# Performance work log

Measured on AMD Instinct MI355X. Metric: run time of the kernel, lower is better.

The kernel has to match this reference:

```python
import jax, jax.numpy as jnp
import numpy as np

D_MODEL = 1024
NUM_HEADS = 16
D_K = D_MODEL // NUM_HEADS


def setup_inputs() -> dict:
    key = jax.random.key(0)
    ks = jax.random.split(key, 3)
    B, S = 4, 2048
    x = jax.random.normal(ks[0], (B, S, D_MODEL), dtype=jnp.float32)
    mask = jnp.ones((1, 1, S, S), dtype=jnp.int32)
    # xavier-uniform-ish init for weights, zeros for biases (matches _reset_parameters)
    lim_qkv = float(np.sqrt(6.0 / (D_MODEL + 3 * D_MODEL)))
    w_qkv = jax.random.uniform(ks[1], (D_MODEL, 3 * D_MODEL), minval=-lim_qkv, maxval=lim_qkv, dtype=jnp.float32)
    b_qkv = jnp.zeros((3 * D_MODEL,), dtype=jnp.float32)
    lim_out = float(np.sqrt(6.0 / (2 * D_MODEL)))
    w_out = jax.random.uniform(ks[2], (D_MODEL, D_MODEL), minval=-lim_out, maxval=lim_out, dtype=jnp.float32)
    b_out = jnp.zeros((D_MODEL,), dtype=jnp.float32)
    return {"x": x, "mask": mask, "w_qkv": w_qkv, "b_qkv": b_qkv, "w_out": w_out, "b_out": b_out}


def reference(x, mask, w_qkv, b_qkv, w_out, b_out):
    B, S, _ = x.shape
    qkv = x @ w_qkv + b_qkv                      # [B,S,3D]
    q, k, v = jnp.split(qkv, 3, axis=-1)         # each [B,S,D]

    def split_heads(t):
        return t.reshape(B, S, NUM_HEADS, D_K).transpose(0, 2, 1, 3)  # [B,H,S,Dk]

    q, k, v = split_heads(q), split_heads(k), split_heads(v)
    scores = jnp.einsum('bhqd,bhkd->bhqk', q, k) / jnp.sqrt(jnp.float32(D_K))
    scores = jnp.where(mask == 0, jnp.float32(-jnp.inf), scores)
    attn = jax.nn.softmax(scores, axis=-1)
    out = jnp.einsum('bhqk,bhkd->bhqd', attn, v)  # [B,H,S,Dk]
    out = out.transpose(0, 2, 1, 3).reshape(B, S, D_MODEL)
    return out @ w_out + b_out
```

## Files before the change

### kernel.cpp

```cpp
#include <hip/hip_runtime.h>
#include <hip/hip_bf16.h>

typedef __bf16 bf16x8 __attribute__((ext_vector_type(8)));
typedef float f32x4 __attribute__((ext_vector_type(4)));
typedef unsigned int u32x4 __attribute__((ext_vector_type(4)));
typedef unsigned short u16;
typedef unsigned int u32;

__device__ __forceinline__ u16 f2bf(float f) {
    union { float f; u32 u; } v; v.f = f;
    u32 r = v.u + 0x7fffu + ((v.u >> 16) & 1u);
    return (u16)(r >> 16);
}

__device__ __forceinline__ u32 cvtpk(float lo, float hi) {
    u32 r;
    asm("v_cvt_pk_bf16_f32 %0, %1, %2" : "=v"(r) : "v"(lo), "v"(hi));
    return r;
}

__device__ __forceinline__ void swap16(u32& a, u32& b) {
    asm("v_permlane16_swap_b32 %0, %1" : "+v"(a), "+v"(b));
}
__device__ __forceinline__ void swap32(u32& a, u32& b) {
    asm("v_permlane32_swap_b32 %0, %1" : "+v"(a), "+v"(b));
}

#define MFMA(a, b, c) __builtin_amdgcn_mfma_f32_16x16x32_bf16((a), (b), (c), 0, 0, 0)

#define GLOAD16(g, l)                                                          \
    __builtin_amdgcn_global_load_lds(                                          \
        (const __attribute__((address_space(1))) u32*)(g),                     \
        (__attribute__((address_space(3))) u32*)(l), 16, 0, 0)

#define QSCALE 0.18033688011112042f

__global__ __launch_bounds__(256) void k_transpose_w(const float* __restrict__ src,
                                                     u16* __restrict__ dst, int K, int N) {
    __shared__ float tile[32][33];
    int n0 = blockIdx.x * 32, k0 = blockIdx.y * 32;
    int tx = threadIdx.x, ty = threadIdx.y;
#pragma unroll
    for (int i = 0; i < 4; i++)
        tile[ty + i * 8][tx] = src[(k0 + ty + i * 8) * N + n0 + tx];
    __syncthreads();
#pragma unroll
    for (int i = 0; i < 4; i++)
        dst[(n0 + ty + i * 8) * K + k0 + tx] = f2bf(tile[tx][ty + i * 8]);
}

__global__ __launch_bounds__(256) void k_cvt_x(const float* __restrict__ X,
                                               u16* __restrict__ Xb) {
    int i = blockIdx.x * 256 + threadIdx.x;
    float4 a = *(const float4*)&X[i * 8];
    float4 b = *(const float4*)&X[i * 8 + 4];
    uint4 o;
    o.x = cvtpk(a.x, a.y);
    o.y = cvtpk(a.z, a.w);
    o.z = cvtpk(b.x, b.y);
    o.w = cvtpk(b.z, b.w);
    *(uint4*)&Xb[i * 8] = o;
}

__global__ __launch_bounds__(256) void k_gemm_qkv(const u16* __restrict__ Xb,
                                                  const u16* __restrict__ Wt,
                                                  const float* __restrict__ bias,
                                                  u16* __restrict__ Qb,
                                                  u16* __restrict__ Kb,
                                                  u16* __restrict__ Vt) {
    __shared__ __align__(16) u16 Asw[128 * 64];
    __shared__ __align__(16) u16 Bsw[128 * 64];
    const int K = 1024;
    int m0 = blockIdx.x * 128, n0 = blockIdx.y * 128;
    int tid = threadIdx.x, lane = tid & 63, w = tid >> 6;
    int wm = w >> 1, wn = w & 1;
    int l15 = lane & 15, l4 = lane >> 4;

    f32x4 z = {0.f, 0.f, 0.f, 0.f};
    f32x4 acc[4][4];
#pragma unroll
    for (int i = 0; i < 4; i++)
#pragma unroll
        for (int j = 0; j < 4; j++) acc[i][j] = z;

    for (int kt = 0; kt < K / 64; kt++) {
#pragma unroll
        for (int it = 0; it < 4; it++) {
            int c = tid + it * 256;
            int row = c >> 3, g = (c & 7) ^ (row & 7);
            GLOAD16(&Xb[(m0 + row) * K + kt * 64 + g * 8], &Asw[(c & ~63) * 8]);
            GLOAD16(&Wt[(n0 + row) * K + kt * 64 + g * 8], &Bsw[(c & ~63) * 8]);
        }
        __syncthreads();
#pragma unroll
        for (int ks = 0; ks < 2; ks++) {
            bf16x8 af[4], bfr[4];
#pragma unroll
            for (int mt = 0; mt < 4; mt++) {
                int row = wm * 64 + mt * 16 + l15;
                af[mt] = *(const bf16x8*)&Asw[row * 64 + ((ks * 4 + l4) ^ (row & 7)) * 8];
            }
#pragma unroll
            for (int nt = 0; nt < 4; nt++) {
                int row = wn * 64 + nt * 16 + l15;
                bfr[nt] = *(const bf16x8*)&Bsw[row * 64 + ((ks * 4 + l4) ^ (row & 7)) * 8];
            }
#pragma unroll
            for (int mt = 0; mt < 4; mt++)
#pragma unroll
                for (int nt = 0; nt < 4; nt++)
                    acc[mt][nt] = MFMA(af[mt], bfr[nt], acc[mt][nt]);
        }
        __syncthreads();
    }
    int part = n0 >> 10;
#pragma unroll
    for (int nt = 0; nt < 4; nt++) {
        int col = n0 + wn * 64 + nt * 16 + l15;
        float bv = bias[col];
        int cc = col & 1023, h = cc >> 6, dk = cc & 63;
        if (part == 2) {
#pragma unroll
            for (int mt = 0; mt < 4; mt++) {
                int row = m0 + wm * 64 + mt * 16 + l4 * 4;
                int b = row >> 11, s = row & 2047;
                uint2 pk;
                pk.x = cvtpk(acc[mt][nt][0] + bv, acc[mt][nt][1] + bv);
                pk.y = cvtpk(acc[mt][nt][2] + bv, acc[mt][nt][3] + bv);
                *(uint2*)&Vt[((b * 16 + h) * 64 + dk) * 2048 + s] = pk;
            }
        } else {
            u16* dst = (part == 0) ? Qb : Kb;
            float sc = (part == 0) ? QSCALE : 1.0f;
#pragma unroll
            for (int mt = 0; mt < 4; mt++) {
#pragma unroll
                for (int q = 0; q < 4; q++) {
                    int row = m0 + wm * 64 + mt * 16 + l4 * 4 + q;
                    int b = row >> 11, s = row & 2047;
                    float v = (acc[mt][nt][q] + bv) * sc;
                    dst[((b * 16 + h) * 2048 + s) * 64 + dk] = f2bf(v);
                }
            }
        }
    }
}

__global__ __launch_bounds__(512) void k_attn(const u16* __restrict__ Qb,
                                              const u16* __restrict__ Kb,
                                              const u16* __restrict__ Vt,
                                              u16* __restrict__ Ob) {
    __shared__ __align__(16) u16 Ksw[2 * 128 * 64];
    __shared__ __align__(16) u16 Vsw[2 * 128 * 64];
    const int S = 2048;
    int bid = blockIdx.x;
    int nbid = (bid & 7) * 64 + (bid >> 3);
    int bh = nbid >> 3;
    int qblk = nbid & 7;
    int b = bh >> 4, h = bh & 15;
    int tid = threadIdx.x, lane = tid & 63, w = tid >> 6;
    int l15 = lane & 15, l4 = lane >> 4, l7 = l15 & 7;
    int q0 = qblk * 256 + w * 32;

    const u16* KbB = Kb + bh * S * 64;
    const u16* VtB = Vt + bh * 64 * S;

    bf16x8 qf[2][2];
#pragma unroll
    for (int mt = 0; mt < 2; mt++)
#pragma unroll
        for (int ks = 0; ks < 2; ks++)
            qf[mt][ks] = *(const bf16x8*)&Qb[(bh * S + q0 + mt * 16 + l15) * 64 + ks * 32 + l4 * 8];

    const f32x4 z = {0.f, 0.f, 0.f, 0.f};
    f32x4 o[2][4];
    f32x4 ol[2];
#pragma unroll
    for (int mt = 0; mt < 2; mt++) {
        ol[mt] = z;
#pragma unroll
        for (int nt = 0; nt < 4; nt++) o[mt][nt] = z;
    }
    union { u32x4 u; bf16x8 bb; } onesu;
    onesu.u = (u32x4){0x3F803F80u, 0x3F803F80u, 0x3F803F80u, 0x3F803F80u};
    const bf16x8 onesf = onesu.bb;

    auto stage = [&](int buf, int kv0) {
#pragma unroll
        for (int it = 0; it < 2; it++) {
            int c = tid + it * 512;
            {
                int row = c >> 3, g = (c & 7) ^ (row & 7);
                GLOAD16(&KbB[(kv0 + row) * 64 + g * 8], &Ksw[buf * 8192 + (c & ~63) * 8]);
            }
            {
                int half = c >> 9, row = (c >> 3) & 63, g = (c & 7) ^ (row & 7);
                GLOAD16(&VtB[row * S + kv0 + half * 64 + g * 8], &Vsw[buf * 8192 + (c & ~63) * 8]);
            }
        }
    };

    stage(0, 0);
    __syncthreads();

    for (int kv = 0; kv < S / 128; kv++) {
        int cur = kv & 1;
        if (kv + 1 < S / 128) stage(cur ^ 1, (kv + 1) * 128);
        const u16* Kc = &Ksw[cur * 8192];
        const u16* Vc = &Vsw[cur * 8192];

#pragma unroll
        for (int half = 0; half < 2; half++) {
            const u16* Kh = Kc + half * 4096;
            const u16* Vh = Vc + half * 4096;

            f32x4 sa[2][4];
            __builtin_amdgcn_s_setprio(1);
            {
                bf16x8 kf[4];
#pragma unroll
                for (int nt = 0; nt < 4; nt++)
                    kf[nt] = *(const bf16x8*)&Kh[(nt * 16 + l15) * 64 + (l4 ^ l7) * 8];
#pragma unroll
                for (int mt = 0; mt < 2; mt++)
#pragma unroll
                    for (int nt = 0; nt < 4; nt++)
                        sa[mt][nt] = MFMA(kf[nt], qf[mt][0], z);
#pragma unroll
                for (int nt = 0; nt < 4; nt++)
                    kf[nt] = *(const bf16x8*)&Kh[(nt * 16 + l15) * 64 + ((4 + l4) ^ l7) * 8];
#pragma unroll
                for (int mt = 0; mt < 2; mt++)
#pragma unroll
                    for (int nt = 0; nt < 4; nt++)
                        sa[mt][nt] = MFMA(kf[nt], qf[mt][1], sa[mt][nt]);
            }
            __builtin_amdgcn_s_setprio(0);

            bf16x8 pf[2][2];
#pragma unroll
            for (int mt = 0; mt < 2; mt++) {
                u32 a0[4], a1[4];
#pragma unroll
                for (int nt = 0; nt < 4; nt++) {
                    float p0 = __builtin_amdgcn_exp2f(sa[mt][nt][0]);
                    float p1 = __builtin_amdgcn_exp2f(sa[mt][nt][1]);
                    float p2 = __builtin_amdgcn_exp2f(sa[mt][nt][2]);
                    float p3 = __builtin_amdgcn_exp2f(sa[mt][nt][3]);
                    a0[nt] = cvtpk(p0, p1);
                    a1[nt] = cvtpk(p2, p3);
                }
#pragma unroll
                for (int ks = 0; ks < 2; ks++) {
                    u32 x = a0[2 * ks], zz = a0[2 * ks + 1];
                    u32 y = a1[2 * ks], ww = a1[2 * ks + 1];
                    swap32(x, zz);
                    swap32(y, ww);
                    swap16(x, zz);
                    swap16(y, ww);
                    union { u32x4 u; bf16x8 bb; } pw;
                    pw.u = (u32x4){x, y, zz, ww};
                    pf[mt][ks] = pw.bb;
                }
            }

            __builtin_amdgcn_s_setprio(1);
#pragma unroll
            for (int ks = 0; ks < 2; ks++) {
                bf16x8 vf[4];
#pragma unroll
                for (int nt = 0; nt < 4; nt++)
                    vf[nt] = *(const bf16x8*)&Vh[(nt * 16 + l15) * 64 + ((ks * 4 + l4) ^ l7) * 8];
#pragma unroll
                for (int mt = 0; mt < 2; mt++) {
#pragma unroll
                    for (int nt = 0; nt < 4; nt++)
                        o[mt][nt] = MFMA(vf[nt], pf[mt][ks], o[mt][nt]);
                    ol[mt] = MFMA(onesf, pf[mt][ks], ol[mt]);
                }
            }
            __builtin_amdgcn_s_setprio(0);
        }
        __syncthreads();
    }

#pragma unroll
    for (int mt = 0; mt < 2; mt++) {
        float inv = 1.f / ol[mt][0];
        int q = q0 + mt * 16 + l15;
#pragma unroll
        for (int nt = 0; nt < 4; nt++) {
            uint2 pk;
            pk.x = cvtpk(o[mt][nt][0] * inv, o[mt][nt][1] * inv);
            pk.y = cvtpk(o[mt][nt][2] * inv, o[mt][nt][3] * inv);
            *(uint2*)&Ob[(b * 2048 + q) * 1024 + h * 64 + nt * 16 + l4 * 4] = pk;
        }
    }
}

__global__ __launch_bounds__(256) void k_gemm_out(const u16* __restrict__ A,
                                                  const u16* __restrict__ Wt,
                                                  const float* __restrict__ bias,
                                                  float* __restrict__ out) {
    __shared__ __align__(16) u16 Asw[128 * 64];
    __shared__ __align__(16) u16 Bsw[128 * 64];
    const int K = 1024, N = 1024;
    int m0 = blockIdx.x * 128, n0 = blockIdx.y * 128;
    int tid = threadIdx.x, lane = tid & 63, w = tid >> 6;
    int wm = w >> 1, wn = w & 1;
    int l15 = lane & 15, l4 = lane >> 4;

    f32x4 z = {0.f, 0.f, 0.f, 0.f};
    f32x4 acc[4][4];
#pragma unroll
    for (int i = 0; i < 4; i++)
#pragma unroll
        for (int j = 0; j < 4; j++) acc[i][j] = z;

    for (int kt = 0; kt < K / 64; kt++) {
#pragma unroll
        for (int it = 0; it < 4; it++) {
            int c = tid + it * 256;
            int row = c >> 3, g = (c & 7) ^ (row & 7);
            GLOAD16(&A[(m0 + row) * K + kt * 64 + g * 8], &Asw[(c & ~63) * 8]);
            GLOAD16(&Wt[(n0 + row) * K + kt * 64 + g * 8], &Bsw[(c & ~63) * 8]);
        }
        __syncthreads();
#pragma unroll
        for (int ks = 0; ks < 2; ks++) {
            bf16x8 af[4], bfr[4];
#pragma unroll
            for (int mt = 0; mt < 4; mt++) {
                int row = wm * 64 + mt * 16 + l15;
                af[mt] = *(const bf16x8*)&Asw[row * 64 + ((ks * 4 + l4) ^ (row & 7)) * 8];
            }
#pragma unroll
            for (int nt = 0; nt < 4; nt++) {
                int row = wn * 64 + nt * 16 + l15;
                bfr[nt] = *(const bf16x8*)&Bsw[row * 64 + ((ks * 4 + l4) ^ (row & 7)) * 8];
            }
#pragma unroll
            for (int mt = 0; mt < 4; mt++)
#pragma unroll
                for (int nt = 0; nt < 4; nt++)
                    acc[mt][nt] = MFMA(af[mt], bfr[nt], acc[mt][nt]);
        }
        __syncthreads();
    }
#pragma unroll
    for (int nt = 0; nt < 4; nt++) {
        int col = n0 + wn * 64 + nt * 16 + l15;
        float bv = bias[col];
#pragma unroll
        for (int mt = 0; mt < 4; mt++) {
#pragma unroll
            for (int q = 0; q < 4; q++) {
                int row = m0 + wm * 64 + mt * 16 + l4 * 4 + q;
                out[row * N + col] = acc[mt][nt][q] + bv;
            }
        }
    }
}

extern "C" void kernel_launch(void* const* d_in, const int* in_sizes, int n_in,
                              void* d_out, int out_size, void* d_ws, size_t ws_size,
                              hipStream_t stream) {
    (void)in_sizes; (void)n_in; (void)out_size; (void)ws_size;
    const float* x     = (const float*)d_in[0];
    const float* w_qkv = (const float*)d_in[2];
    const float* b_qkv = (const float*)d_in[3];
    const float* w_out = (const float*)d_in[4];
    const float* b_out = (const float*)d_in[5];
    float* out = (float*)d_out;

    char* ws = (char*)d_ws;
    u16* WqkvT = (u16*)(ws + 0);
    u16* WoT   = (u16*)(ws + 6291456);
    u16* Qb    = (u16*)(ws + 8388608);
    u16* Kb    = (u16*)(ws + 25165824);
    u16* Xb    = (u16*)(ws + 41943040);
    u16* Ob    = Xb;
    u16* Vt    = (u16*)(ws + 58720256);

    k_transpose_w<<<dim3(96, 32), dim3(32, 8), 0, stream>>>(w_qkv, WqkvT, 1024, 3072);
    k_transpose_w<<<dim3(32, 32), dim3(32, 8), 0, stream>>>(w_out, WoT, 1024, 1024);
    k_cvt_x<<<dim3(4096), 256, 0, stream>>>(x, Xb);
    k_gemm_qkv<<<dim3(64, 24), 256, 0, stream>>>(Xb, WqkvT, b_qkv, Qb, Kb, Vt);
    k_attn<<<dim3(512), 512, 0, stream>>>(Qb, Kb, Vt, Ob);
    k_gemm_out<<<dim3(64, 8), 256, 0, stream>>>(Ob, WoT, b_out, out);
}
```

Baseline: 181.9 us.

## Merge prep kernels into one launch and shrink attention KV tile to 64

Folds the two weight-transpose launches and the x-to-bf16 conversion into one k_prep kernel that dispatches on block index, removing two launches and their gaps. The attention kernel now stages 64-key tiles instead of 128, halving shared memory per block so more blocks can be resident, but it issues twice as many barriers and stage iterations. The smaller LDS footprint may help occupancy, while the extra synchronization per key could cost throughput.

```diff
diff --git a/kernel.cpp b/kernel.cpp
--- a/kernel.cpp
+++ b/kernel.cpp
@@ -35,11 +35,41 @@
 
 #define QSCALE 0.18033688011112042f
 
-__global__ __launch_bounds__(256) void k_transpose_w(const float* __restrict__ src,
-                                                     u16* __restrict__ dst, int K, int N) {
+__global__ __launch_bounds__(256) void k_prep(const float* __restrict__ x,
+                                              u16* __restrict__ Xb,
+                                              const float* __restrict__ w_qkv,
+                                              u16* __restrict__ WqkvT,
+                                              const float* __restrict__ w_out,
+                                              u16* __restrict__ WoT) {
     __shared__ float tile[32][33];
-    int n0 = blockIdx.x * 32, k0 = blockIdx.y * 32;
-    int tx = threadIdx.x, ty = threadIdx.y;
+    int bid = blockIdx.x;
+    int tid = threadIdx.x;
+    if (bid < 4096) {
+        int i = bid * 256 + tid;
+        float4 a = *(const float4*)&x[i * 8];
+        float4 b = *(const float4*)&x[i * 8 + 4];
+        uint4 o;
+        o.x = cvtpk(a.x, a.y);
+        o.y = cvtpk(a.z, a.w);
+        o.z = cvtpk(b.x, b.y);
+        o.w = cvtpk(b.z, b.w);
+        *(uint4*)&Xb[i * 8] = o;
+        return;
+    }
+    const float* src;
+    u16* dst;
+    int n0, k0, N;
+    if (bid < 4096 + 3072) {
+        int t = bid - 4096;
+        src = w_qkv; dst = WqkvT; N = 3072;
+        n0 = (t % 96) * 32; k0 = (t / 96) * 32;
+    } else {
+        int t = bid - 7168;
+        src = w_out; dst = WoT; N = 1024;
+        n0 = (t & 31) * 32; k0 = (t >> 5) * 32;
+    }
+    const int K = 1024;
+    int tx = tid & 31, ty = tid >> 5;
 #pragma unroll
     for (int i = 0; i < 4; i++)
         tile[ty + i * 8][tx] = src[(k0 + ty + i * 8) * N + n0 + tx];
@@ -47,19 +77,6 @@
 #pragma unroll
     for (int i = 0; i < 4; i++)
         dst[(n0 + ty + i * 8) * K + k0 + tx] = f2bf(tile[tx][ty + i * 8]);
-}
-
-__global__ __launch_bounds__(256) void k_cvt_x(const float* __restrict__ X,
-                                               u16* __restrict__ Xb) {
-    int i = blockIdx.x * 256 + threadIdx.x;
-    float4 a = *(const float4*)&X[i * 8];
-    float4 b = *(const float4*)&X[i * 8 + 4];
-    uint4 o;
-    o.x = cvtpk(a.x, a.y);
-    o.y = cvtpk(a.z, a.w);
-    o.z = cvtpk(b.x, b.y);
-    o.w = cvtpk(b.z, b.w);
-    *(uint4*)&Xb[i * 8] = o;
 }
 
 __global__ __launch_bounds__(256) void k_gemm_qkv(const u16* __restrict__ Xb,
@@ -150,8 +167,8 @@
                                               const u16* __restrict__ Kb,
                                               const u16* __restrict__ Vt,
                                               u16* __restrict__ Ob) {
-    __shared__ __align__(16) u16 Ksw[2 * 128 * 64];
-    __shared__ __align__(16) u16 Vsw[2 * 128 * 64];
+    __shared__ __align__(16) u16 Ksw[2 * 64 * 64];
+    __shared__ __align__(16) u16 Vsw[2 * 64 * 64];
     const int S = 2048;
     int bid = blockIdx.x;
     int nbid = (bid & 7) * 64 + (bid >> 3);
@@ -186,101 +203,87 @@
     const bf16x8 onesf = onesu.bb;
 
     auto stage = [&](int buf, int kv0) {
-#pragma unroll
-        for (int it = 0; it < 2; it++) {
-            int c = tid + it * 512;
-            {
-                int row = c >> 3, g = (c & 7) ^ (row & 7);
-                GLOAD16(&KbB[(kv0 + row) * 64 + g * 8], &Ksw[buf * 8192 + (c & ~63) * 8]);
-            }
-            {
-                int half = c >> 9, row = (c >> 3) & 63, g = (c & 7) ^ (row & 7);
-                GLOAD16(&VtB[row * S + kv0 + half * 64 + g * 8], &Vsw[buf * 8192 + (c & ~63) * 8]);
-            }
-        }
+        int c = tid;
+        int row = c >> 3, g = (c & 7) ^ (row & 7);
+        GLOAD16(&KbB[(kv0 + row) * 64 + g * 8], &Ksw[buf * 4096 + (c & ~63) * 8]);
+        GLOAD16(&VtB[row * S + kv0 + g * 8], &Vsw[buf * 4096 + (c & ~63) * 8]);
     };
 
     stage(0, 0);
     __syncthreads();
 
-    for (int kv = 0; kv < S / 128; kv++) {
+    for (int kv = 0; kv < S / 64; kv++) {
         int cur = kv & 1;
-        if (kv + 1 < S / 128) stage(cur ^ 1, (kv + 1) * 128);
-        const u16* Kc = &Ksw[cur * 8192];
-        const u16* Vc = &Vsw[cur * 8192];
-
-#pragma unroll
-        for (int half = 0; half < 2; half++) {
-            const u16* Kh = Kc + half * 4096;
-            const u16* Vh = Vc + half * 4096;
-
-            f32x4 sa[2][4];
-            __builtin_amdgcn_s_setprio(1);
-            {
-                bf16x8 kf[4];
-#pragma unroll
-                for (int nt = 0; nt < 4; nt++)
-                    kf[nt] = *(const bf16x8*)&Kh[(nt * 16 + l15) * 64 + (l4 ^ l7) * 8];
-#pragma unroll
-                for (int mt = 0; mt < 2; mt++)
-#pragma unroll
-                    for (int nt = 0; nt < 4; nt++)
-                        sa[mt][nt] = MFMA(kf[nt], qf[mt][0], z);
-#pragma unroll
-                for (int nt = 0; nt < 4; nt++)
-                    kf[nt] = *(const bf16x8*)&Kh[(nt * 16 + l15) * 64 + ((4 + l4) ^ l7) * 8];
-#pragma unroll
-                for (int mt = 0; mt < 2; mt++)
-#pragma unroll
-                    for (int nt = 0; nt < 4; nt++)
-                        sa[mt][nt] = MFMA(kf[nt], qf[mt][1], sa[mt][nt]);
-            }
-            __builtin_amdgcn_s_setprio(0);
-
-            bf16x8 pf[2][2];
+        if (kv + 1 < S / 64) stage(cur ^ 1, (kv + 1) * 64);
+        const u16* Kc = &Ksw[cur * 4096];
+        const u16* Vc = &Vsw[cur * 4096];
+
+        f32x4 sa[2][4];
+        __builtin_amdgcn_s_setprio(1);
+        {
+            bf16x8 kf[4];
+#pragma unroll
+            for (int nt = 0; nt < 4; nt++)
+                kf[nt] = *(const bf16x8*)&Kc[(nt * 16 + l15) * 64 + (l4 ^ l7) * 8];
+#pragma unroll
+            for (int mt = 0; mt < 2; mt++)
+#pragma unroll
+                for (int nt = 0; nt < 4; nt++)
+                    sa[mt][nt] = MFMA(kf[nt], qf[mt][0], z);
+#pragma unroll
+            for (int nt = 0; nt < 4; nt++)
+                kf[nt] = *(const bf16x8*)&Kc[(nt * 16 + l15) * 64 + ((4 + l4) ^ l7) * 8];
+#pragma unroll
+            for (int mt = 0; mt < 2; mt++)
+#pragma unroll
+                for (int nt = 0; nt < 4; nt++)
+                    sa[mt][nt] = MFMA(kf[nt], qf[mt][1], sa[mt][nt]);
+        }
+        __builtin_amdgcn_s_setprio(0);
+
+        bf16x8 pf[2][2];
+#pragma unroll
+        for (int mt = 0; mt < 2; mt++) {
+            u32 a0[4], a1[4];
+#pragma unroll
+            for (int nt = 0; nt < 4; nt++) {
+                float p0 = __builtin_amdgcn_exp2f(sa[mt][nt][0]);
+                float p1 = __builtin_amdgcn_exp2f(sa[mt][nt][1]);
+                float p2 = __builtin_amdgcn_exp2f(sa[mt][nt][2]);
+                float p3 = __builtin_amdgcn_exp2f(sa[mt][nt][3]);
+                a0[nt] = cvtpk(p0, p1);
+                a1[nt] = cvtpk(p2, p3);
+            }
+#pragma unroll
+            for (int ks = 0; ks < 2; ks++) {
+                u32 x = a0[2 * ks], zz = a0[2 * ks + 1];
+                u32 y = a1[2 * ks], ww = a1[2 * ks + 1];
+                swap32(x, zz);
+                swap32(y, ww);
+                swap16(x, zz);
+                swap16(y, ww);
+                union { u32x4 u; bf16x8 bb; } pw;
+                pw.u = (u32x4){x, y, zz, ww};
+                pf[mt][ks] = pw.bb;
+            }
+        }
+
+        __builtin_amdgcn_s_setprio(1);
+#pragma unroll
+        for (int ks = 0; ks < 2; ks++) {
+            bf16x8 vf[4];
+#pragma unroll
+            for (int nt = 0; nt < 4; nt++)
+                vf[nt] = *(const bf16x8*)&Vc[(nt * 16 + l15) * 64 + ((ks * 4 + l4) ^ l7) * 8];
 #pragma unroll
             for (int mt = 0; mt < 2; mt++) {
-                u32 a0[4], a1[4];
-#pragma unroll
-                for (int nt = 0; nt < 4; nt++) {
-                    float p0 = __builtin_amdgcn_exp2f(sa[mt][nt][0]);
-                    float p1 = __builtin_amdgcn_exp2f(sa[mt][nt][1]);
-                    float p2 = __builtin_amdgcn_exp2f(sa[mt][nt][2]);
-                    float p3 = __builtin_amdgcn_exp2f(sa[mt][nt][3]);
-                    a0[nt] = cvtpk(p0, p1);
-                    a1[nt] = cvtpk(p2, p3);
-                }
-#pragma unroll
-                for (int ks = 0; ks < 2; ks++) {
-                    u32 x = a0[2 * ks], zz = a0[2 * ks + 1];
-                    u32 y = a1[2 * ks], ww = a1[2 * ks + 1];
-                    swap32(x, zz);
-                    swap32(y, ww);
-                    swap16(x, zz);
-                    swap16(y, ww);
-                    union { u32x4 u; bf16x8 bb; } pw;
-                    pw.u = (u32x4){x, y, zz, ww};
-                    pf[mt][ks] = pw.bb;
-                }
-            }
-
-            __builtin_amdgcn_s_setprio(1);
-#pragma unroll
-            for (int ks = 0; ks < 2; ks++) {
-                bf16x8 vf[4];
-#pragma unroll
-                for (int nt = 0; nt < 4; nt++)
-                    vf[nt] = *(const bf16x8*)&Vh[(nt * 16 + l15) * 64 + ((ks * 4 + l4) ^ l7) * 8];
-#pragma unroll
-                for (int mt = 0; mt < 2; mt++) {
-#pragma unroll
-                    for (int nt = 0; nt < 4; nt++)
-                        o[mt][nt] = MFMA(vf[nt], pf[mt][ks], o[mt][nt]);
-                    ol[mt] = MFMA(onesf, pf[mt][ks], ol[mt]);
-                }
-            }
-            __builtin_amdgcn_s_setprio(0);
-        }
+#pragma unroll
+                for (int nt = 0; nt < 4; nt++)
+                    o[mt][nt] = MFMA(vf[nt], pf[mt][ks], o[mt][nt]);
+                ol[mt] = MFMA(onesf, pf[mt][ks], ol[mt]);
+            }
+        }
+        __builtin_amdgcn_s_setprio(0);
         __syncthreads();
     }
 
@@ -382,9 +385,7 @@
     u16* Ob    = Xb;
     u16* Vt    = (u16*)(ws + 58720256);
 
-    k_transpose_w<<<dim3(96, 32), dim3(32, 8), 0, stream>>>(w_qkv, WqkvT, 1024, 3072);
-    k_transpose_w<<<dim3(32, 32), dim3(32, 8), 0, stream>>>(w_out, WoT, 1024, 1024);
-    k_cvt_x<<<dim3(4096), 256, 0, stream>>>(x, Xb);
+    k_prep<<<dim3(8192), 256, 0, stream>>>(x, Xb, w_qkv, WqkvT, w_out, WoT);
     k_gemm_qkv<<<dim3(64, 24), 256, 0, stream>>>(Xb, WqkvT, b_qkv, Qb, Kb, Vt);
     k_attn<<<dim3(512), 512, 0, stream>>>(Qb, Kb, Vt, Ob);
     k_gemm_out<<<dim3(64, 8), 256, 0, stream>>>(Ob, WoT, b_out, out);
```

Result: faster. 172.7 us (median of 2 runs) (-5.0%).
